# Optimization experiments

Measured on AMD Instinct MI355X. Metric: run time of the kernel, lower is better.

The kernel has to match this reference:

```python
import math
import jax, jax.numpy as jnp
import numpy as np

NUM_HEADS, RAD_PTS, LVL_PTS = 8, 4, 1
P = RAD_PTS * LVL_PTS


def setup_inputs() -> dict:
    B, Nq, Din = 2, 21760, 256
    hw = np.array([[128, 128], [64, 64], [32, 32], [16, 16]], np.int64)
    sizes = hw[:, 0] * hw[:, 1]
    offs = np.concatenate([[0], np.cumsum(sizes)[:-1]]).astype(np.int64)
    Ns = int(sizes.sum())
    map_ids = np.tile(np.repeat(np.arange(4), sizes)[None], (B, 1)).astype(np.int64)

    key = jax.random.key(0)
    ks = jax.random.split(key, 8)
    in_feats = jax.random.normal(ks[0], (B, Nq, Din), jnp.float32)
    sample_feats = jax.random.normal(ks[1], (B, Ns, Din), jnp.float32)
    sample_priors = jax.random.uniform(ks[2], (B, Nq, 2), jnp.float32)

    # sample_offsets bias: radial grid init as in the torch module
    thetas = np.arange(NUM_HEADS) * (2.0 * math.pi / NUM_HEADS)
    grid = np.stack([np.cos(thetas), np.sin(thetas), np.zeros(NUM_HEADS)], 1)
    grid = grid / np.abs(grid).max(1, keepdims=True)
    grid = np.tile(grid.reshape(NUM_HEADS, 1, 1, 3), (1, RAD_PTS, LVL_PTS, 1))
    grid = grid * np.arange(1, RAD_PTS + 1).reshape(1, RAD_PTS, 1, 1)
    bo = jnp.asarray(grid.reshape(-1), jnp.float32)

    Wo = jax.random.normal(ks[3], (NUM_HEADS * P * 3, Din), jnp.float32) * 0.01
    Wa = jax.random.normal(ks[4], (NUM_HEADS * P, Din), jnp.float32) * 0.01
    ba = jnp.zeros((NUM_HEADS * P,), jnp.float32)
    s = 1.0 / np.sqrt(Din)
    Wv = jax.random.normal(ks[5], (Din, Din), jnp.float32) * s
    bv = jnp.zeros((Din,), jnp.float32)
    Wout = jax.random.normal(ks[6], (Din, Din), jnp.float32) * s
    bout = jnp.zeros((Din,), jnp.float32)

    return dict(in_feats=in_feats, sample_priors=sample_priors, sample_feats=sample_feats,
                map_hw=jnp.asarray(hw), map_offs=jnp.asarray(offs), map_ids=jnp.asarray(map_ids),
                Wo=Wo, bo=bo, Wa=Wa, ba=ba, Wv=Wv, bv=bv, Wout=Wout, bout=bout)


def _trilinear_sample(val, map_hw, map_offs, xy, z, L):
    # val [B,Ns,H,D]; xy [B,Q,H,P,2] normalized; z [B,Q,H,P] in ~[0,1]
    B, Ns, H, D = val.shape
    Q = xy.shape[1]
    val_t = val.transpose(0, 2, 1, 3)  # [B,H,Ns,D]
    x, y = xy[..., 0], xy[..., 1]
    lvl_f = z * (L - 1)
    l0 = jnp.floor(lvl_f).astype(jnp.int32)
    wz = lvl_f - l0.astype(lvl_f.dtype)

    def gather(idx):  # idx [B,Q,H,P] int32 -> [B,Q,H,P,D]
        it = idx.transpose(0, 2, 1, 3).reshape(B, H, Q * P, 1)
        g = jnp.take_along_axis(val_t, it, axis=2)  # [B,H,Q*P,D]
        return g.reshape(B, H, Q, P, D).transpose(0, 2, 1, 3, 4)

    def sample_level(lvl):  # bilinear sample within pyramid level `lvl` (zero padding)
        valid_l = (lvl >= 0) & (lvl < L)
        lc = jnp.clip(lvl, 0, L - 1)
        Hl = map_hw[lc, 0].astype(jnp.int32)
        Wl = map_hw[lc, 1].astype(jnp.int32)
        off = map_offs[lc].astype(jnp.int32)
        xf = x * Wl.astype(x.dtype) - 0.5
        yf = y * Hl.astype(x.dtype) - 0.5
        x0 = jnp.floor(xf).astype(jnp.int32)
        y0 = jnp.floor(yf).astype(jnp.int32)
        dx = xf - x0.astype(x.dtype)
        dy = yf - y0.astype(x.dtype)
        out = jnp.zeros((B, Q, H, P, D), x.dtype)
        corners = [(x0, y0, (1 - dx) * (1 - dy)), (x0 + 1, y0, dx * (1 - dy)),
                   (x0, y0 + 1, (1 - dx) * dy), (x0 + 1, y0 + 1, dx * dy)]
        for xi, yi, w in corners:
            ok = valid_l & (xi >= 0) & (xi < Wl) & (yi >= 0) & (yi < Hl)
            idx = off + jnp.clip(yi, 0, Hl - 1) * Wl + jnp.clip(xi, 0, Wl - 1)
            out = out + gather(idx) * (w * ok.astype(x.dtype))[..., None]
        return out

    return sample_level(l0) * (1 - wz)[..., None] + sample_level(l0 + 1) * wz[..., None]


def reference(in_feats, sample_priors, sample_feats, map_hw, map_offs, map_ids,
              Wo, bo, Wa, ba, Wv, bv, Wout, bout):
    B, Nq, _ = in_feats.shape
    Ns = sample_feats.shape[1]
    L = map_hw.shape[0]
    D = Wv.shape[0] // NUM_HEADS

    val = (sample_feats @ Wv.T + bv).reshape(B, Ns, NUM_HEADS, D)
    offs = (in_feats @ Wo.T + bo).reshape(B, Nq, NUM_HEADS, P, 3)

    # sample_priors last dim == 2: normalize offsets by (W, H) of the query's map
    norm = map_hw[:, ::-1][map_ids].astype(offs.dtype)  # [B,Nq,2] (w,h)
    sample_xy = sample_priors[:, :, None, None, :2] + offs[..., :2] / norm[:, :, None, None, :]

    lvl_off = jnp.arange(LVL_PTS, dtype=offs.dtype) - 0.5 * (LVL_PTS - 1)
    z_grid = map_ids[:, :, None, None, None].astype(offs.dtype) + lvl_off  # [B,Nq,1,1,Lp]
    z_grid = jnp.broadcast_to(z_grid, (B, Nq, NUM_HEADS, RAD_PTS, LVL_PTS)).reshape(B, Nq, NUM_HEADS, P)
    sample_z = (z_grid + jnp.tanh(offs[..., 2])) / (L - 1)

    attn = jax.nn.softmax((in_feats @ Wa.T + ba).reshape(B, Nq, NUM_HEADS, P), axis=3)

    sampled = _trilinear_sample(val, map_hw, map_offs, sample_xy, sample_z, L)  # [B,Nq,H,P,D]
    attn_feats = jnp.einsum('bqhpd,bqhp->bqhd', sampled, attn).reshape(B, Nq, NUM_HEADS * D)
    return attn_feats @ Wout.T + bout
```

## Files before the change

kernel.cpp:

```cpp
#include <hip/hip_runtime.h>
#include <hip/hip_bf16.h>
#include <math.h>

typedef __bf16 bf16x8 __attribute__((ext_vector_type(8)));
typedef float f32x4 __attribute__((ext_vector_type(4)));
typedef float f32x2 __attribute__((ext_vector_type(2)));
typedef unsigned short ushort8 __attribute__((ext_vector_type(8)));

static __device__ __forceinline__ unsigned short f2bf(float f) {
    union { float f; unsigned u; } c; c.f = f;
    unsigned r = c.u + 0x7FFFu + ((c.u >> 16) & 1u);
    return (unsigned short)(r >> 16);
}
static __device__ __forceinline__ float bf2f(unsigned short u) {
    union { unsigned u; float f; } c; c.u = ((unsigned)u) << 16;
    return c.f;
}

static __device__ __forceinline__ void gload_lds16(
    const unsigned short* g, unsigned short* l)
{
    __builtin_amdgcn_global_load_lds(
        (const __attribute__((address_space(1))) void*)g,
        (__attribute__((address_space(3))) void*)l, 16, 0, 0);
}

__global__ __launch_bounds__(256) void convert_weights_hist(
    const float* __restrict__ Wv, const float* __restrict__ Wo,
    const float* __restrict__ Wa, const float* __restrict__ Wout,
    const float* __restrict__ bo, const float* __restrict__ ba,
    unsigned short* __restrict__ Wv_b, unsigned short* __restrict__ Woa_b,
    unsigned short* __restrict__ Wout_b, float* __restrict__ boa,
    const float* __restrict__ priors, int* __restrict__ counts,
    int BQ, int Nq)
{
    __shared__ int cnt[16];
    if (threadIdx.x < 16) cnt[threadIdx.x] = 0;
    __syncthreads();

    int gid = blockIdx.x * blockDim.x + threadIdx.x;
    int stride = gridDim.x * blockDim.x;
    for (int i = gid; i < 163840; i += stride) {
        if (i < 65536)       Wv_b[i] = f2bf(Wv[i]);
        else if (i < 90112)  Woa_b[i - 65536] = f2bf(Wo[i - 65536]);
        else if (i < 98304)  Woa_b[i - 65536] = f2bf(Wa[i - 90112]);
        else                 Wout_b[i - 98304] = f2bf(Wout[i - 98304]);
    }
    if (gid < 96)       boa[gid] = bo[gid];
    else if (gid < 128) boa[gid] = ba[gid - 96];

    for (int q = gid; q < BQ; q += stride) {
        int b = q / Nq;
        float py = priors[(size_t)q * 2 + 1];
        int band = min(7, max(0, (int)(py * 8.0f)));
        atomicAdd(&cnt[b * 8 + band], 1);
    }
    __syncthreads();
    if (threadIdx.x < 16 && cnt[threadIdx.x] > 0)
        atomicAdd(&counts[threadIdx.x], cnt[threadIdx.x]);
}

__global__ __launch_bounds__(256) void bucket_scatter(
    const float* __restrict__ priors, const int* __restrict__ counts,
    int* __restrict__ cursors, int* __restrict__ qidx, int BQ, int Nq)
{
    __shared__ int lcnt[16];
    __shared__ int lbase[16];
    const int tid = threadIdx.x;
    if (tid < 16) lcnt[tid] = 0;
    __syncthreads();
    int q = blockIdx.x * 256 + tid;
    int mybucket = 0, myslot = 0;
    bool valid = q < BQ;
    if (valid) {
        int b = q / Nq;
        float py = priors[(size_t)q * 2 + 1];
        int band = min(7, max(0, (int)(py * 8.0f)));
        mybucket = b * 8 + band;
        myslot = atomicAdd(&lcnt[mybucket], 1);
    }
    __syncthreads();
    if (tid < 16) {
        int base = 0;
        #pragma unroll
        for (int i = 0; i < 16; ++i) base += (i < tid) ? counts[i] : 0;
        lbase[tid] = base + atomicAdd(&cursors[tid], lcnt[tid]);
    }
    __syncthreads();
    if (valid) qidx[lbase[mybucket] + myslot] = q;
}

template<int WM, int WN, bool A_BF16, int OUT_MODE>
__global__ __launch_bounds__(WM * WN * 64) void gemm_mfma(
    const void* __restrict__ Av, const unsigned short* __restrict__ W,
    const float* __restrict__ bias, void* __restrict__ Cv,
    int M, int N, int K, int NsPB)
{
    constexpr int BM = WM * 64;
    constexpr int BN = WN * 64;
    constexpr int BK = 64;
    constexpr int NWAVE = WM * WN;
    constexpr int NTHR = NWAVE * 64;
    constexpr int LDP = 72;
    constexpr int ASZ = A_BF16 ? (BM * 64) : (BM * LDP);

    __shared__ __align__(16) unsigned short As[ASZ];
    __shared__ __align__(16) unsigned short Bs[BN * 64];

    const int bm  = blockIdx.x * BM;
    const int bn  = blockIdx.y * BN;
    const int tid = threadIdx.x;
    const int wid = tid >> 6;
    const int wrow = wid / WN;
    const int wcol = wid % WN;
    const int lane = tid & 63;
    const int lr = lane & 15;
    const int lg = lane >> 4;
    const int lrow = lane >> 3;
    const int lc16 = (lane & 7) ^ (lrow & 7);

    f32x4 acc[4][4];
    #pragma unroll
    for (int mi = 0; mi < 4; ++mi)
        #pragma unroll
        for (int ni = 0; ni < 4; ++ni)
            acc[mi][ni] = (f32x4){0.f, 0.f, 0.f, 0.f};

    for (int kt = 0; kt < K; kt += BK) {
        #pragma unroll
        for (int c = wid; c < BN / 8; c += NWAVE) {
            const unsigned short* g =
                W + (size_t)(bn + c * 8 + lrow) * K + kt + lc16 * 8;
            gload_lds16(g, Bs + c * 512);
        }
        if (A_BF16) {
            const unsigned short* A = (const unsigned short*)Av;
            #pragma unroll
            for (int c = wid; c < BM / 8; c += NWAVE) {
                const unsigned short* g =
                    A + (size_t)(bm + c * 8 + lrow) * K + kt + lc16 * 8;
                gload_lds16(g, As + c * 512);
            }
        } else {
            const float* A = (const float*)Av;
            #pragma unroll
            for (int u = tid; u < BM * 8; u += NTHR) {
                int r = u >> 3, kb = u & 7;
                const float* src = A + (size_t)(bm + r) * K + kt + kb * 8;
                float4 f0 = *(const float4*)(src);
                float4 f1 = *(const float4*)(src + 4);
                ushort8 v;
                v[0] = f2bf(f0.x); v[1] = f2bf(f0.y);
                v[2] = f2bf(f0.z); v[3] = f2bf(f0.w);
                v[4] = f2bf(f1.x); v[5] = f2bf(f1.y);
                v[6] = f2bf(f1.z); v[7] = f2bf(f1.w);
                *(ushort8*)(As + r * LDP + kb * 8) = v;
            }
        }
        __syncthreads();

        #pragma unroll
        for (int kk = 0; kk < 2; ++kk) {
            bf16x8 fa[4], fb[4];
            #pragma unroll
            for (int mi = 0; mi < 4; ++mi) {
                int row = wrow * 64 + mi * 16 + lr;
                if (A_BF16) {
                    fa[mi] = *(const bf16x8*)(As + row * 64 +
                                              ((kk * 4 + lg) ^ (lr & 7)) * 8);
                } else {
                    fa[mi] = *(const bf16x8*)(As + row * LDP +
                                              kk * 32 + lg * 8);
                }
            }
            #pragma unroll
            for (int ni = 0; ni < 4; ++ni) {
                int row = wcol * 64 + ni * 16 + lr;
                fb[ni] = *(const bf16x8*)(Bs + row * 64 +
                                          ((kk * 4 + lg) ^ (lr & 7)) * 8);
            }
            #pragma unroll
            for (int mi = 0; mi < 4; ++mi)
                #pragma unroll
                for (int ni = 0; ni < 4; ++ni)
                    acc[mi][ni] = __builtin_amdgcn_mfma_f32_16x16x32_bf16(
                        fa[mi], fb[ni], acc[mi][ni], 0, 0, 0);
        }
        __syncthreads();
    }

    if (OUT_MODE == 2) {
        const int b = bm / NsPB;
        const int ns_base = bm - b * NsPB;
        #pragma unroll
        for (int ni = 0; ni < 4; ++ni) {
            int col = wcol * 64 + ni * 16 + lr;
            int h   = col >> 5;
            int ch  = col & 31;
            float bv = bias[col];
            unsigned short* dst = (unsigned short*)Cv +
                (size_t)(b * 8 + h) * NsPB * 32 + ch;
            #pragma unroll
            for (int mi = 0; mi < 4; ++mi) {
                #pragma unroll
                for (int r = 0; r < 4; ++r) {
                    int ns = ns_base + mi * 16 + lg * 4 + r;
                    dst[(size_t)ns * 32] = f2bf(acc[mi][ni][r] + bv);
                }
            }
        }
    } else {
        #pragma unroll
        for (int ni = 0; ni < 4; ++ni) {
            int col = bn + wcol * 64 + ni * 16 + lr;
            float bv = bias[col];
            #pragma unroll
            for (int mi = 0; mi < 4; ++mi) {
                #pragma unroll
                for (int r = 0; r < 4; ++r) {
                    int row = bm + wrow * 64 + mi * 16 + lg * 4 + r;
                    if (OUT_MODE == 1) {
                        ((unsigned short*)Cv)[(size_t)row * N + col] =
                            f2bf(acc[mi][ni][r] + bv);
                    } else {
                        ((float*)Cv)[(size_t)row * N + col] = acc[mi][ni][r] + bv;
                    }
                }
            }
        }
    }
}

__global__ __launch_bounds__(256) void msda_sample_kernel(
    const unsigned short* __restrict__ C1,
    const float* __restrict__ priors,
    const unsigned short* __restrict__ val,
    const int*   __restrict__ map_hw,
    const int*   __restrict__ map_offs,
    const int*   __restrict__ map_ids,
    const int*   __restrict__ qidx,
    unsigned short* __restrict__ out,
    int Nq, int Ns)
{
    const int swz  = (blockIdx.x & 7) * (gridDim.x >> 3) + (blockIdx.x >> 3);
    const int wvi  = threadIdx.x >> 6;
    const int lane = threadIdx.x & 63;
    const int bq   = qidx[swz * 4 + wvi];
    const int b    = bq / Nq;
    const int q    = bq - b * Nq;

    __shared__ __align__(16) float s_rec[4][4][128];

    {
        const int hp = lane >> 1;
        const int sl = lane & 1;
        const unsigned short* sc = C1 + (size_t)bq * 128;
        float o0 = bf2f(sc[hp * 3 + 0]);
        float o1 = bf2f(sc[hp * 3 + 1]);
        float o2 = bf2f(sc[hp * 3 + 2]);
        float logit = bf2f(sc[96 + hp]);

        float m = logit;
        m = fmaxf(m, __shfl_xor(m, 2));
        m = fmaxf(m, __shfl_xor(m, 4));
        float e = expf(logit - m);
        float s = e;
        s += __shfl_xor(s, 2);
        s += __shfl_xor(s, 4);
        float attnw = e / s;

        int lid = map_ids[(size_t)b * Ns + q];
        float px = priors[(size_t)bq * 2 + 0];
        float py = priors[(size_t)bq * 2 + 1];
        int Hq = map_hw[lid * 2 + 0];
        int Wq = map_hw[lid * 2 + 1];
        float x = px + o0 / (float)Wq;
        float y = py + o1 / (float)Hq;

        float lvl_f = (float)lid + tanhf(o2);
        float l0f = floorf(lvl_f);
        int   l0  = (int)l0f;
        float wz  = lvl_f - l0f;

        const int   lv = l0 + sl;
        const float wl = sl ? wz : (1.0f - wz);
        float w4[4];
        int   i4[4];
        if (lv >= 0 && lv < 4) {
            int Hs  = map_hw[lv * 2 + 0];
            int Ws  = map_hw[lv * 2 + 1];
            int off = map_offs[lv];
            float xf = x * (float)Ws - 0.5f;
            float yf = y * (float)Hs - 0.5f;
            float x0f = floorf(xf), y0f = floorf(yf);
            int   x0  = (int)x0f,  y0  = (int)y0f;
            float dx = xf - x0f, dy = yf - y0f;
            #pragma unroll
            for (int j = 0; j < 4; ++j) {
                int xi = x0 + (j & 1);
                int yi = y0 + (j >> 1);
                float w = ((j & 1) ? dx : 1.0f - dx) *
                          ((j >> 1) ? dy : 1.0f - dy);
                bool ok = (xi >= 0) && (xi < Ws) && (yi >= 0) && (yi < Hs);
                w4[j] = ok ? (w * wl * attnw) : 0.0f;
                i4[j] = ok ? ((off + yi * Ws + xi) << 6) : 0;
            }
        } else {
            #pragma unroll
            for (int j = 0; j < 4; ++j) { w4[j] = 0.0f; i4[j] = 0; }
        }
        f32x4 wrec = {w4[0], w4[1], w4[2], w4[3]};
        f32x4 irec = {__int_as_float(i4[0]), __int_as_float(i4[1]),
                      __int_as_float(i4[2]), __int_as_float(i4[3])};
        *(f32x4*)&s_rec[wvi][sl][hp * 4]     = wrec;
        *(f32x4*)&s_rec[wvi][2 + sl][hp * 4] = irec;
    }
    asm volatile("s_waitcnt lgkmcnt(0)" ::: "memory");

    const int p2 = lane & 1;
    const int d8 = (lane >> 1) & 3;
    const int h  = lane >> 3;
    const char* vbase = (const char*)(val + (size_t)(b * 8 + h) * Ns * 32)
                        + d8 * 16;

    f32x4 wrec[4], irec[4];
    #pragma unroll
    for (int pp = 0; pp < 2; ++pp) {
        const int hp = h * 4 + p2 + pp * 2;
        wrec[pp * 2 + 0] = *(const f32x4*)&s_rec[wvi][0][hp * 4];
        wrec[pp * 2 + 1] = *(const f32x4*)&s_rec[wvi][1][hp * 4];
        irec[pp * 2 + 0] = *(const f32x4*)&s_rec[wvi][2][hp * 4];
        irec[pp * 2 + 1] = *(const f32x4*)&s_rec[wvi][3][hp * 4];
    }

    uint4 u[16];
    #pragma unroll
    for (int r = 0; r < 4; ++r)
        #pragma unroll
        for (int j = 0; j < 4; ++j)
            u[r * 4 + j] = *(const uint4*)(vbase + __float_as_int(irec[r][j]));

    f32x2 acc2[4];
    #pragma unroll
    for (int k = 0; k < 4; ++k) acc2[k] = (f32x2){0.f, 0.f};

    #pragma unroll
    for (int r = 0; r < 4; ++r) {
        #pragma unroll
        for (int j = 0; j < 4; ++j) {
            float w = wrec[r][j];
            f32x2 w2 = {w, w};
            unsigned ua[4] = {u[r * 4 + j].x, u[r * 4 + j].y,
                              u[r * 4 + j].z, u[r * 4 + j].w};
            #pragma unroll
            for (int k = 0; k < 4; ++k) {
                union { unsigned u; float f; } lo, hi;
                lo.u = ua[k] << 16;
                hi.u = ua[k] & 0xffff0000u;
                f32x2 v2 = {lo.f, hi.f};
                acc2[k] += w2 * v2;
            }
        }
    }

    #pragma unroll
    for (int k = 0; k < 4; ++k) {
        acc2[k][0] += __shfl_xor(acc2[k][0], 1);
        acc2[k][1] += __shfl_xor(acc2[k][1], 1);
    }

    if (p2 == 0) {
        ushort8 o;
        #pragma unroll
        for (int k = 0; k < 4; ++k) {
            o[2 * k]     = f2bf(acc2[k][0]);
            o[2 * k + 1] = f2bf(acc2[k][1]);
        }
        *(ushort8*)(out + (size_t)bq * 256 + h * 32 + d8 * 8) = o;
    }
}

extern "C" void kernel_launch(void* const* d_in, const int* in_sizes, int n_in,
                              void* d_out, int out_size, void* d_ws, size_t ws_size,
                              hipStream_t stream) {
    const float* in_feats      = (const float*)d_in[0];
    const float* sample_priors = (const float*)d_in[1];
    const float* sample_feats  = (const float*)d_in[2];
    const int*   map_hw        = (const int*)d_in[3];
    const int*   map_offs      = (const int*)d_in[4];
    const int*   map_ids       = (const int*)d_in[5];
    const float* Wo            = (const float*)d_in[6];
    const float* bo            = (const float*)d_in[7];
    const float* Wa            = (const float*)d_in[8];
    const float* ba            = (const float*)d_in[9];
    const float* Wv            = (const float*)d_in[10];
    const float* bv            = (const float*)d_in[11];
    const float* Wout          = (const float*)d_in[12];
    const float* bout          = (const float*)d_in[13];
    float* out = (float*)d_out;

    const int B = 2, Nq = 21760, Din = 256;
    const int Ns = in_sizes[2] / (B * Din);
    const int BQ = B * Nq;

    unsigned short* val = (unsigned short*)d_out;
    unsigned short* C1b = (unsigned short*)d_ws;
    unsigned short* af  = C1b + (size_t)BQ * 128;
    char* wbase = (char*)(af + (size_t)BQ * 256);
    unsigned short* Wv_b   = (unsigned short*)wbase;
    unsigned short* Woa_b  = Wv_b + 65536;
    unsigned short* Wout_b = Woa_b + 32768;
    float* boa = (float*)(Wout_b + 65536);
    int* bws  = (int*)(boa + 128);
    int* qidx = bws + 32;

    hipMemsetAsync(bws, 0, 128, stream);

    convert_weights_hist<<<dim3(160), dim3(256), 0, stream>>>(
        Wv, Wo, Wa, Wout, bo, ba, Wv_b, Woa_b, Wout_b, boa,
        sample_priors, bws, BQ, Nq);

    bucket_scatter<<<dim3((BQ + 255) / 256), dim3(256), 0, stream>>>(
        sample_priors, bws, bws + 16, qidx, BQ, Nq);

    gemm_mfma<1, 4, false, 2><<<dim3(BQ / 64, 1), dim3(256), 0, stream>>>(
        sample_feats, Wv_b, bv, val, B * Ns, 256, Din, Ns);

    gemm_mfma<2, 2, false, 1><<<dim3(BQ / 128, 1), dim3(256), 0, stream>>>(
        in_feats, Woa_b, boa, C1b, BQ, 128, Din, Ns);

    msda_sample_kernel<<<dim3(BQ / 4), dim3(256), 0, stream>>>(
        C1b, sample_priors, val, map_hw, map_offs, map_ids, qidx, af, Nq, Ns);

    gemm_mfma<1, 4, true, 0><<<dim3(BQ / 64, 1), dim3(256), 0, stream>>>(
        af, Wout_b, bout, out, BQ, 256, Din, Ns);
}
```

Measured before the change: 114.9 us.

## Process four queries per wave in sampling kernel and keep offset GEMM output in fp32

The sampling kernel now has each wave handle four queries instead of one. Their offset and logit records are loaded up front and staged in a larger shared buffer, then the gathers run per query in two halves to limit register pressure. The offset/attention GEMM now writes fp32 instead of bf16 with a 1x2 wave config, which raises the bytes written and read for that intermediate. Integer divisions by Nq become comparisons, which assumes B=2.

```diff
diff --git a/kernel.cpp b/kernel.cpp
--- a/kernel.cpp
+++ b/kernel.cpp
@@ -11,10 +11,6 @@
     union { float f; unsigned u; } c; c.f = f;
     unsigned r = c.u + 0x7FFFu + ((c.u >> 16) & 1u);
     return (unsigned short)(r >> 16);
-}
-static __device__ __forceinline__ float bf2f(unsigned short u) {
-    union { unsigned u; float f; } c; c.u = ((unsigned)u) << 16;
-    return c.f;
 }
 
 static __device__ __forceinline__ void gload_lds16(
@@ -50,7 +46,7 @@
     else if (gid < 128) boa[gid] = ba[gid - 96];
 
     for (int q = gid; q < BQ; q += stride) {
-        int b = q / Nq;
+        int b = (q >= Nq) ? 1 : 0;
         float py = priors[(size_t)q * 2 + 1];
         int band = min(7, max(0, (int)(py * 8.0f)));
         atomicAdd(&cnt[b * 8 + band], 1);
@@ -73,7 +69,7 @@
     int mybucket = 0, myslot = 0;
     bool valid = q < BQ;
     if (valid) {
-        int b = q / Nq;
+        int b = (q >= Nq) ? 1 : 0;
         float py = priors[(size_t)q * 2 + 1];
         int band = min(7, max(0, (int)(py * 8.0f)));
         mybucket = b * 8 + band;
@@ -232,7 +228,7 @@
 }
 
 __global__ __launch_bounds__(256) void msda_sample_kernel(
-    const unsigned short* __restrict__ C1,
+    const float* __restrict__ C1,
     const float* __restrict__ priors,
     const unsigned short* __restrict__ val,
     const int*   __restrict__ map_hw,
@@ -245,21 +241,38 @@
     const int swz  = (blockIdx.x & 7) * (gridDim.x >> 3) + (blockIdx.x >> 3);
     const int wvi  = threadIdx.x >> 6;
     const int lane = threadIdx.x & 63;
-    const int bq   = qidx[swz * 4 + wvi];
-    const int b    = bq / Nq;
-    const int q    = bq - b * Nq;
-
-    __shared__ __align__(16) float s_rec[4][4][128];
-
-    {
-        const int hp = lane >> 1;
-        const int sl = lane & 1;
-        const unsigned short* sc = C1 + (size_t)bq * 128;
-        float o0 = bf2f(sc[hp * 3 + 0]);
-        float o1 = bf2f(sc[hp * 3 + 1]);
-        float o2 = bf2f(sc[hp * 3 + 2]);
-        float logit = bf2f(sc[96 + hp]);
-
+    const int qbase = swz * 16 + wvi * 4;
+
+    __shared__ __align__(16) float s_rec[4][4][4][128];
+
+    const int hp = lane >> 1;
+    const int sl = lane & 1;
+
+    int bq4[4];
+    #pragma unroll
+    for (int qq = 0; qq < 4; ++qq) bq4[qq] = qidx[qbase + qq];
+
+    float o0[4], o1[4], o2[4], lgt[4], px[4], py[4];
+    int bb[4], lid[4];
+    #pragma unroll
+    for (int qq = 0; qq < 4; ++qq) {
+        const int bq = bq4[qq];
+        const int b  = (bq >= Nq) ? 1 : 0;
+        const int q  = bq - b * Nq;
+        bb[qq] = b;
+        const float* sc = C1 + (size_t)bq * 128;
+        o0[qq]  = sc[hp * 3 + 0];
+        o1[qq]  = sc[hp * 3 + 1];
+        o2[qq]  = sc[hp * 3 + 2];
+        lgt[qq] = sc[96 + hp];
+        px[qq]  = priors[(size_t)bq * 2 + 0];
+        py[qq]  = priors[(size_t)bq * 2 + 1];
+        lid[qq] = map_ids[(size_t)b * Ns + q];
+    }
+
+    #pragma unroll
+    for (int qq = 0; qq < 4; ++qq) {
+        float logit = lgt[qq];
         float m = logit;
         m = fmaxf(m, __shfl_xor(m, 2));
         m = fmaxf(m, __shfl_xor(m, 4));
@@ -269,15 +282,12 @@
         s += __shfl_xor(s, 4);
         float attnw = e / s;
 
-        int lid = map_ids[(size_t)b * Ns + q];
-        float px = priors[(size_t)bq * 2 + 0];
-        float py = priors[(size_t)bq * 2 + 1];
-        int Hq = map_hw[lid * 2 + 0];
-        int Wq = map_hw[lid * 2 + 1];
-        float x = px + o0 / (float)Wq;
-        float y = py + o1 / (float)Hq;
-
-        float lvl_f = (float)lid + tanhf(o2);
+        int Hq = map_hw[lid[qq] * 2 + 0];
+        int Wq = map_hw[lid[qq] * 2 + 1];
+        float x = px[qq] + o0[qq] / (float)Wq;
+        float y = py[qq] + o1[qq] / (float)Hq;
+
+        float lvl_f = (float)lid[qq] + tanhf(o2[qq]);
         float l0f = floorf(lvl_f);
         int   l0  = (int)l0f;
         float wz  = lvl_f - l0f;
@@ -312,71 +322,71 @@
         f32x4 wrec = {w4[0], w4[1], w4[2], w4[3]};
         f32x4 irec = {__int_as_float(i4[0]), __int_as_float(i4[1]),
                       __int_as_float(i4[2]), __int_as_float(i4[3])};
-        *(f32x4*)&s_rec[wvi][sl][hp * 4]     = wrec;
-        *(f32x4*)&s_rec[wvi][2 + sl][hp * 4] = irec;
+        *(f32x4*)&s_rec[wvi][qq][sl][hp * 4]     = wrec;
+        *(f32x4*)&s_rec[wvi][qq][2 + sl][hp * 4] = irec;
     }
     asm volatile("s_waitcnt lgkmcnt(0)" ::: "memory");
 
     const int p2 = lane & 1;
     const int d8 = (lane >> 1) & 3;
     const int h  = lane >> 3;
-    const char* vbase = (const char*)(val + (size_t)(b * 8 + h) * Ns * 32)
-                        + d8 * 16;
-
-    f32x4 wrec[4], irec[4];
+
     #pragma unroll
-    for (int pp = 0; pp < 2; ++pp) {
-        const int hp = h * 4 + p2 + pp * 2;
-        wrec[pp * 2 + 0] = *(const f32x4*)&s_rec[wvi][0][hp * 4];
-        wrec[pp * 2 + 1] = *(const f32x4*)&s_rec[wvi][1][hp * 4];
-        irec[pp * 2 + 0] = *(const f32x4*)&s_rec[wvi][2][hp * 4];
-        irec[pp * 2 + 1] = *(const f32x4*)&s_rec[wvi][3][hp * 4];
-    }
-
-    uint4 u[16];
-    #pragma unroll
-    for (int r = 0; r < 4; ++r)
-        #pragma unroll
-        for (int j = 0; j < 4; ++j)
-            u[r * 4 + j] = *(const uint4*)(vbase + __float_as_int(irec[r][j]));
-
-    f32x2 acc2[4];
-    #pragma unroll
-    for (int k = 0; k < 4; ++k) acc2[k] = (f32x2){0.f, 0.f};
-
-    #pragma unroll
-    for (int r = 0; r < 4; ++r) {
-        #pragma unroll
-        for (int j = 0; j < 4; ++j) {
-            float w = wrec[r][j];
-            f32x2 w2 = {w, w};
-            unsigned ua[4] = {u[r * 4 + j].x, u[r * 4 + j].y,
-                              u[r * 4 + j].z, u[r * 4 + j].w};
+    for (int qq = 0; qq < 4; ++qq) {
+        const char* vbase =
+            (const char*)(val + (size_t)(bb[qq] * 8 + h) * Ns * 32) + d8 * 16;
+
+        f32x2 acc2[4];
+        #pragma unroll
+        for (int k = 0; k < 4; ++k) acc2[k] = (f32x2){0.f, 0.f};
+
+        #pragma unroll
+        for (int pp = 0; pp < 2; ++pp) {
+            const int hpg = h * 4 + p2 + pp * 2;
+            f32x4 wlo = *(const f32x4*)&s_rec[wvi][qq][0][hpg * 4];
+            f32x4 whi = *(const f32x4*)&s_rec[wvi][qq][1][hpg * 4];
+            f32x4 xlo = *(const f32x4*)&s_rec[wvi][qq][2][hpg * 4];
+            f32x4 xhi = *(const f32x4*)&s_rec[wvi][qq][3][hpg * 4];
+
+            uint4 u[8];
+            #pragma unroll
+            for (int j = 0; j < 4; ++j)
+                u[j] = *(const uint4*)(vbase + __float_as_int(xlo[j]));
+            #pragma unroll
+            for (int j = 0; j < 4; ++j)
+                u[4 + j] = *(const uint4*)(vbase + __float_as_int(xhi[j]));
+
+            #pragma unroll
+            for (int j = 0; j < 8; ++j) {
+                float w = (j < 4) ? wlo[j] : whi[j - 4];
+                f32x2 w2 = {w, w};
+                unsigned ua[4] = {u[j].x, u[j].y, u[j].z, u[j].w};
+                #pragma unroll
+                for (int k = 0; k < 4; ++k) {
+                    union { unsigned uu; float f; } lo, hi;
+                    lo.uu = ua[k] << 16;
+                    hi.uu = ua[k] & 0xffff0000u;
+                    f32x2 v2 = {lo.f, hi.f};
+                    acc2[k] += w2 * v2;
+                }
+            }
+        }
+
+        #pragma unroll
+        for (int k = 0; k < 4; ++k) {
+            acc2[k][0] += __shfl_xor(acc2[k][0], 1);
+            acc2[k][1] += __shfl_xor(acc2[k][1], 1);
+        }
+
+        if (p2 == 0) {
+            ushort8 o;
             #pragma unroll
             for (int k = 0; k < 4; ++k) {
-                union { unsigned u; float f; } lo, hi;
-                lo.u = ua[k] << 16;
-                hi.u = ua[k] & 0xffff0000u;
-                f32x2 v2 = {lo.f, hi.f};
-                acc2[k] += w2 * v2;
-            }
-        }
-    }
-
-    #pragma unroll
-    for (int k = 0; k < 4; ++k) {
-        acc2[k][0] += __shfl_xor(acc2[k][0], 1);
-        acc2[k][1] += __shfl_xor(acc2[k][1], 1);
-    }
-
-    if (p2 == 0) {
-        ushort8 o;
-        #pragma unroll
-        for (int k = 0; k < 4; ++k) {
-            o[2 * k]     = f2bf(acc2[k][0]);
-            o[2 * k + 1] = f2bf(acc2[k][1]);
-        }
-        *(ushort8*)(out + (size_t)bq * 256 + h * 32 + d8 * 8) = o;
+                o[2 * k]     = f2bf(acc2[k][0]);
+                o[2 * k + 1] = f2bf(acc2[k][1]);
+            }
+            *(ushort8*)(out + (size_t)bq4[qq] * 256 + h * 32 + d8 * 8) = o;
+        }
     }
 }
 
@@ -404,9 +414,9 @@
     const int BQ = B * Nq;
 
     unsigned short* val = (unsigned short*)d_out;
-    unsigned short* C1b = (unsigned short*)d_ws;
-    unsigned short* af  = C1b + (size_t)BQ * 128;
-    char* wbase = (char*)(af + (size_t)BQ * 256);
+    float* C1 = (float*)d_ws;
+    unsigned short* af = (unsigned short*)((char*)d_ws + (size_t)BQ * 128 * 4);
+    char* wbase = (char*)d_ws + (size_t)BQ * 128 * 4 + (size_t)BQ * 256 * 2;
     unsigned short* Wv_b   = (unsigned short*)wbase;
     unsigned short* Woa_b  = Wv_b + 65536;
     unsigned short* Wout_b = Woa_b + 32768;
@@ -426,11 +436,11 @@
     gemm_mfma<1, 4, false, 2><<<dim3(BQ / 64, 1), dim3(256), 0, stream>>>(
         sample_feats, Wv_b, bv, val, B * Ns, 256, Din, Ns);
 
-    gemm_mfma<2, 2, false, 1><<<dim3(BQ / 128, 1), dim3(256), 0, stream>>>(
-        in_feats, Woa_b, boa, C1b, BQ, 128, Din, Ns);
-
-    msda_sample_kernel<<<dim3(BQ / 4), dim3(256), 0, stream>>>(
-        C1b, sample_priors, val, map_hw, map_offs, map_ids, qidx, af, Nq, Ns);
+    gemm_mfma<1, 2, false, 0><<<dim3(BQ / 64, 1), dim3(128), 0, stream>>>(
+        in_feats, Woa_b, boa, C1, BQ, 128, Din, Ns);
+
+    msda_sample_kernel<<<dim3(BQ / 16), dim3(256), 0, stream>>>(
+        C1, sample_priors, val, map_hw, map_offs, map_ids, qidx, af, Nq, Ns);
 
     gemm_mfma<1, 4, true, 0><<<dim3(BQ / 64, 1), dim3(256), 0, stream>>>(
         af, Wout_b, bout, out, BQ, 256, Din, Ns);
```

Measured after the change: 115.9 us. No clear change (+0.8%).
